# Kernel tuning notes

Hardware: AMD Instinct MI355X
Metric: run time of the kernel (lower is better)

Reference implementation:

```python
import jax, jax.numpy as jnp
import numpy as np

NP_, NA_ = 50000, 20000
D_IN, D_HID, D_OUT = 128, 128, 64
E_W, E_C, E_R = 250000, 500000, 250000


def setup_inputs() -> dict:
    key = jax.random.key(0)
    ks = jax.random.split(key, 14)
    s_in = 1.0 / np.sqrt(D_IN)
    s_h = 1.0 / np.sqrt(D_HID)
    return {
        "x_paper": jax.random.normal(ks[0], (NP_, D_IN), jnp.float32),
        "x_author": jax.random.normal(ks[1], (NA_, D_IN), jnp.float32),
        "Wl1": jax.random.normal(ks[2], (3, D_HID, D_IN), jnp.float32) * s_in,
        "bl1": jax.random.normal(ks[3], (3, D_HID), jnp.float32) * 0.01,
        "Wr1": jax.random.normal(ks[4], (3, D_HID, D_IN), jnp.float32) * s_in,
        "Wl2": jax.random.normal(ks[5], (3, D_OUT, D_HID), jnp.float32) * s_h,
        "bl2": jax.random.normal(ks[6], (3, D_OUT), jnp.float32) * 0.01,
        "Wr2": jax.random.normal(ks[7], (3, D_OUT, D_HID), jnp.float32) * s_h,
        "writes_src": jax.random.randint(ks[8], (E_W,), 0, NA_),
        "writes_dst": jax.random.randint(ks[9], (E_W,), 0, NP_),
        "cites_src": jax.random.randint(ks[10], (E_C,), 0, NP_),
        "cites_dst": jax.random.randint(ks[11], (E_C,), 0, NP_),
        "rev_src": jax.random.randint(ks[12], (E_R,), 0, NP_),
        "rev_dst": jax.random.randint(ks[13], (E_R,), 0, NA_),
    }


def _sage(x_src, x_dst, src, dst, Wl, bl, Wr, n_dst):
    # PyG SAGEConv(aggr='mean'): lin_l(mean_j x_src[j]) + lin_r(x_dst)
    agg = jax.ops.segment_sum(x_src[src], dst, num_segments=n_dst)
    cnt = jax.ops.segment_sum(jnp.ones_like(dst, dtype=x_src.dtype), dst,
                              num_segments=n_dst)
    agg = agg / jnp.maximum(cnt, 1.0)[:, None]  # degree-0 nodes -> 0 (PyG scatter-mean)
    return agg @ Wl.T + bl + x_dst @ Wr.T


def reference(x_paper, x_author, Wl1, bl1, Wr1, Wl2, bl2, Wr2,
              writes_src, writes_dst, cites_src, cites_dst, rev_src, rev_dst):
    def hetero_layer(xp, xa, Wl, bl, Wr):
        # HeteroConv(aggr='mean'): average per-relation outputs per dst node type
        op = 0.5 * (_sage(xa, xp, writes_src, writes_dst, Wl[0], bl[0], Wr[0], NP_)
                    + _sage(xp, xp, cites_src, cites_dst, Wl[1], bl[1], Wr[1], NP_))
        oa = _sage(xp, xa, rev_src, rev_dst, Wl[2], bl[2], Wr[2], NA_)
        return op, oa

    hp, ha = hetero_layer(x_paper, x_author, Wl1, bl1, Wr1)
    hp, ha = jax.nn.relu(hp), jax.nn.relu(ha)  # norm_type='none', dropout eval-mode
    hp, _ = hetero_layer(hp, ha, Wl2, bl2, Wr2)
    return hp  # logits for category='paper', [NP_, D_OUT]
```

## Files before the change

kernel.cpp:

```cpp
#include <hip/hip_runtime.h>

#define NP 50000
#define NA 20000
#define E_W 250000
#define E_C 500000
#define E_R 250000
#define E_TOT (E_W + E_C + E_R)
#define CAP 48
#define RBLK 4096
#define NSEG 245
#define PNODES 15000
#define CHK 500
#define NCH 30
#define NBIN 240

typedef __attribute__((ext_vector_type(8))) short short8;
typedef __attribute__((ext_vector_type(4))) float floatx4;
typedef __attribute__((ext_vector_type(2))) float floatx2;

__device__ __forceinline__ unsigned short f2bf(float f) {
    unsigned u = __float_as_uint(f);
    return (unsigned short)((u + 0x7FFFu + ((u >> 16) & 1u)) >> 16);
}
__device__ __forceinline__ float bflo(unsigned v) { return __uint_as_float(v << 16); }
__device__ __forceinline__ float bfhi(unsigned v) { return __uint_as_float(v & 0xFFFF0000u); }

__device__ __forceinline__ int node_idx(int node) {
    if (node < 2 * NP) {
        int rel1 = node >= NP;
        int d = node - (rel1 ? NP : 0);
        int p2 = d / 6250;
        return p2 * PNODES + (d - p2 * 6250) + (rel1 ? 6250 : 0);
    }
    int d = node - 2 * NP;
    int p2 = d / 2500;
    return p2 * PNODES + 12500 + (d - p2 * 2500);
}

__device__ __forceinline__ int frag_off(int NT, int j, int n, int k) {
    int t = n >> 4, ln = n & 15;
    int kb = k >> 5, q = (k >> 3) & 3, r = k & 7;
    return (((j * NT + t) * 4 + kb) * 64 + q * 16 + ln) * 8 + r;
}

__device__ __forceinline__ void prep_body(
    int idx,
    const float* __restrict__ xp, const float* __restrict__ xa,
    const float* __restrict__ Wl1, const float* __restrict__ Wr1,
    const float* __restrict__ Wl2, const float* __restrict__ Wr2,
    const float* __restrict__ bl1, const float* __restrict__ bl2,
    unsigned short* __restrict__ xpb, unsigned short* __restrict__ xab,
    unsigned* __restrict__ xp8, unsigned* __restrict__ xa8,
    unsigned short* __restrict__ Wp1, unsigned short* __restrict__ Wa1,
    unsigned short* __restrict__ Wt2, unsigned short* __restrict__ Wr2s,
    float* __restrict__ bias_p1, float* __restrict__ bias_a1,
    float* __restrict__ bias_p2) {
    const int n4p = NP * 32, n4a = NA * 32;
    if (idx < n4p + n4a) {
        const float* s; unsigned short* d; unsigned* d8; int i = idx;
        if (i < n4p) { s = xp; d = xpb; d8 = xp8; }
        else { s = xa; d = xab; d8 = xa8; i -= n4p; }
        float4 v = ((const float4*)s)[i];
        ushort4 u;
        u.x = f2bf(v.x); u.y = f2bf(v.y); u.z = f2bf(v.z); u.w = f2bf(v.w);
        ((ushort4*)d)[i] = u;
        int w = __builtin_amdgcn_cvt_pk_fp8_f32(v.x, v.y, 0, false);
        w = __builtin_amdgcn_cvt_pk_fp8_f32(v.z, v.w, w, true);
        d8[i] = (unsigned)w;
        return;
    }
    int j = idx - (n4p + n4a);
    if (j < 49152) {
        int jj = j >> 14, rem = j & 16383, n = rem >> 7, k = rem & 127;
        float v = (jj == 0)   ? 0.5f * Wl1[rem]
                  : (jj == 1) ? 0.5f * Wl1[16384 + rem]
                              : 0.5f * (Wr1[rem] + Wr1[16384 + rem]);
        Wp1[frag_off(8, jj, n, k)] = f2bf(v);
    } else if (j < 81920) {
        int i2 = j - 49152;
        int jj = i2 >> 14, rem = i2 & 16383, n = rem >> 7, k = rem & 127;
        float v = (jj == 0) ? Wl1[2 * 16384 + rem] : Wr1[2 * 16384 + rem];
        Wa1[frag_off(8, jj, n, k)] = f2bf(v);
    } else if (j < 98304) {
        int i2 = j - 81920;
        int jj = i2 >> 13, rem = i2 & 8191, n = rem >> 7, k = rem & 127;
        float v = 0.5f * Wl2[jj * 8192 + rem];
        Wt2[frag_off(4, jj, n, k)] = f2bf(v);
    } else if (j < 106496) {
        int i2 = j - 98304;
        int n = i2 >> 7, k = i2 & 127;
        float v = 0.5f * (Wr2[i2] + Wr2[8192 + i2]);
        Wr2s[frag_off(4, 0, n, k)] = f2bf(v);
    } else if (j < 106496 + 320) {
        int b = j - 106496;
        if (b < 128) bias_p1[b] = 0.5f * (bl1[b] + bl1[128 + b]);
        else if (b < 256) bias_a1[b - 128] = bl1[256 + b - 128];
        else bias_p2[b - 256] = 0.5f * (bl2[b - 256] + bl2[64 + b - 256]);
    }
}

__device__ __forceinline__ void edge_bin(
    int e, const int* __restrict__ w_src, const int* __restrict__ w_dst,
    const int* __restrict__ c_src, const int* __restrict__ c_dst,
    const int* __restrict__ r_src, const int* __restrict__ r_dst,
    int& bin, int& sub, int& src) {
    bool isC = (e >= E_W) & (e < E_W + E_C);
    bool isR = e >= E_W + E_C;
    const int* db = isR ? r_dst : (isC ? c_dst : w_dst);
    const int* sb = isR ? r_src : (isC ? c_src : w_src);
    int idx = e - (isC ? E_W : 0) - (isR ? (E_W + E_C) : 0);
    int d = db[idx];
    src = sb[idx];
    int p, local;
    if (isR) { p = d / 2500; local = 12500 + d - p * 2500; }
    else { p = d / 6250; local = (d - p * 6250) + (isC ? 6250 : 0); }
    int ch = local / CHK;
    bin = p * NCH + ch;
    sub = local - ch * CHK;
}

__device__ __forceinline__ void route_body(
    int bid, const int* __restrict__ w_src, const int* __restrict__ w_dst,
    const int* __restrict__ c_src, const int* __restrict__ c_dst,
    const int* __restrict__ r_src, const int* __restrict__ r_dst,
    unsigned* __restrict__ seg, int* __restrict__ segoff, int* __restrict__ segcnt,
    int* cnt_s, int* base_s, int* cur_s) {
    int tid = threadIdx.x, lane = tid & 63;
    for (int k = tid; k < NBIN; k += 256) cnt_s[k] = 0;
    __syncthreads();
#pragma unroll 4
    for (int u = 0; u < 16; ++u) {
        int e = bid * RBLK + u * 256 + tid;
        if (e < E_TOT) {
            int bin, sub, src;
            edge_bin(e, w_src, w_dst, c_src, c_dst, r_src, r_dst, bin, sub, src);
            atomicAdd(&cnt_s[bin], 1);
        }
    }
    __syncthreads();
    if (tid < 64) {
        int v[4], tot = 0;
#pragma unroll
        for (int q = 0; q < 4; ++q) {
            int k = tid * 4 + q;
            v[q] = (k < NBIN) ? cnt_s[k] : 0;
            tot += v[q];
        }
        int sc = tot;
#pragma unroll
        for (int ofs = 1; ofs < 64; ofs <<= 1) {
            int t = __shfl_up(sc, ofs, 64);
            if (lane >= ofs) sc += t;
        }
        int run = sc - tot;
#pragma unroll
        for (int q = 0; q < 4; ++q) {
            int k = tid * 4 + q;
            if (k < NBIN) { base_s[k] = run; run += v[q]; }
        }
    }
    __syncthreads();
    for (int k = tid; k < NBIN; k += 256) {
        segoff[bid * NBIN + k] = base_s[k];
        segcnt[bid * NBIN + k] = cnt_s[k];
        cur_s[k] = base_s[k];
    }
    __syncthreads();
    unsigned* segb = seg + (size_t)bid * RBLK;
#pragma unroll 4
    for (int u = 0; u < 16; ++u) {
        int e = bid * RBLK + u * 256 + tid;
        if (e < E_TOT) {
            int bin, sub, src;
            edge_bin(e, w_src, w_dst, c_src, c_dst, r_src, r_dst, bin, sub, src);
            int pos = atomicAdd(&cur_s[bin], 1);
            segb[pos] = (unsigned)src | ((unsigned)sub << 16);
        }
    }
}

__global__ __launch_bounds__(256) void route_prep(
    const float* xp, const float* xa, const float* Wl1, const float* Wr1,
    const float* Wl2, const float* Wr2, const float* bl1, const float* bl2,
    unsigned short* xpb, unsigned short* xab, unsigned* xp8, unsigned* xa8,
    unsigned short* Wp1, unsigned short* Wa1, unsigned short* Wt2, unsigned short* Wr2s,
    float* bias_p1, float* bias_a1, float* bias_p2,
    const int* w_src, const int* w_dst, const int* c_src, const int* c_dst,
    const int* r_src, const int* r_dst,
    unsigned* seg, int* segoff, int* segcnt) {
    __shared__ int cnt_s[NBIN], base_s[NBIN], cur_s[NBIN];
    if ((int)blockIdx.x < NSEG)
        route_body(blockIdx.x, w_src, w_dst, c_src, c_dst, r_src, r_dst,
                   seg, segoff, segcnt, cnt_s, base_s, cur_s);
    else
        prep_body((blockIdx.x - NSEG) * 256 + threadIdx.x, xp, xa, Wl1, Wr1, Wl2, Wr2,
                  bl1, bl2, xpb, xab, xp8, xa8, Wp1, Wa1, Wt2, Wr2s,
                  bias_p1, bias_a1, bias_p2);
}

__global__ __launch_bounds__(256) void fill2c(
    const unsigned* __restrict__ seg, const int* __restrict__ segoff,
    const int* __restrict__ segcnt, int* __restrict__ cnt,
    unsigned short* __restrict__ csr) {
    __shared__ unsigned short rows[CHK * CAP];
    __shared__ int cursor[CHK];
    __shared__ int offs[NSEG], cnts[NSEG];
    int k = blockIdx.x, tid = threadIdx.x;
    for (int s = tid; s < NSEG; s += 256) {
        offs[s] = segoff[s * NBIN + k];
        cnts[s] = segcnt[s * NBIN + k];
    }
    for (int l = tid; l < CHK; l += 256) cursor[l] = 0;
    __syncthreads();
    int grp = tid >> 4, gl = tid & 15;
    for (int s = grp; s < NSEG; s += 16) {
        int n = cnts[s];
        const unsigned* sp = seg + (size_t)s * RBLK + offs[s];
        for (int i = gl; i < n; i += 16) {
            unsigned v = sp[i];
            int sub = v >> 16, src = v & 0xFFFFu;
            int pos = atomicAdd(&cursor[sub], 1);
            if (pos < CAP) rows[sub * CAP + pos] = (unsigned short)src;
        }
    }
    __syncthreads();
    int p = k / NCH, ch = k - p * NCH;
    int gbase = p * PNODES + ch * CHK;
    for (int l = tid; l < CHK; l += 256) cnt[gbase + l] = cursor[l];
    const unsigned* rU = (const unsigned*)rows;
    unsigned* cU = (unsigned*)csr + (size_t)gbase * (CAP / 2);
    for (int i = tid; i < CHK * (CAP / 2); i += 256) cU[i] = rU[i];
}

__global__ void agg_pad(const unsigned* __restrict__ s0, unsigned short* __restrict__ d0,
                        const unsigned* __restrict__ s1, unsigned short* __restrict__ d1,
                        const unsigned* __restrict__ s2, unsigned short* __restrict__ d2,
                        const int* __restrict__ cnt, const unsigned short* __restrict__ csr) {
    int g = blockIdx.x * 8 + (threadIdx.x >> 5);
    int lane = threadIdx.x & 63;
    int sl = lane & 31, hw = lane & 32;
    const unsigned* sp; unsigned short* dst; int node, dummy;
    if (g < NP) { sp = s0; dst = d0; node = g; dummy = NA; }
    else if (g < 2 * NP) { sp = s1; dst = d1; node = g - NP; dummy = NP; }
    else if (g < 2 * NP + NA) { sp = s2; dst = d2; node = g - 2 * NP; dummy = NP; }
    else return;
    int idx = node_idx(g);
    int deg = cnt[idx];
    int degc = deg < CAP ? deg : CAP;
    const unsigned short* row = csr + (size_t)idx * CAP;
    int ei0 = (sl < degc) ? (int)row[sl] : dummy;
    int ei1 = (32 + sl < degc) ? (int)row[32 + sl] : dummy;
    int degw = degc;
    int other = __shfl_xor(degw, 32, 64);
    if (other > degw) degw = other;
    float a0 = 0.f, a1 = 0.f, a2 = 0.f, a3 = 0.f;
    float b0 = 0.f, b1 = 0.f, b2 = 0.f, b3 = 0.f;
    for (int i = 0; i < degw; i += 8) {
        unsigned v[8];
#pragma unroll
        for (int u = 0; u < 8; ++u) {
            int ii = i + u;
            int esrc = (ii < 32) ? ei0 : ei1;
            int qq = __shfl(esrc, hw | (ii & 31), 64);
            qq = (ii < degc) ? qq : dummy;
            v[u] = sp[(size_t)qq * 32 + sl];
        }
#pragma unroll
        for (int u = 0; u < 8; ++u) {
            floatx2 lo = __builtin_amdgcn_cvt_pk_f32_fp8(v[u], false);
            floatx2 hi = __builtin_amdgcn_cvt_pk_f32_fp8(v[u], true);
            if (u & 1) { b0 += lo.x; b1 += lo.y; b2 += hi.x; b3 += hi.y; }
            else       { a0 += lo.x; a1 += lo.y; a2 += hi.x; a3 += hi.y; }
        }
    }
    float scl = deg > 0 ? 1.f / (float)deg : 0.f;
    float r0 = (a0 + b0) * scl, r1 = (a1 + b1) * scl;
    float r2 = (a2 + b2) * scl, r3 = (a3 + b3) * scl;
    unsigned wlo = ((unsigned)f2bf(r1) << 16) | (unsigned)f2bf(r0);
    unsigned whi = ((unsigned)f2bf(r3) << 16) | (unsigned)f2bf(r2);
    ((uint2*)dst)[(size_t)node * 32 + sl] = make_uint2(wlo, whi);
}

__global__ void agg2(const unsigned short* __restrict__ ta, const unsigned short* __restrict__ tp,
                     const int* __restrict__ cnt, const unsigned short* __restrict__ csr,
                     float* __restrict__ aggF) {
    int node = blockIdx.x * 8 + (threadIdx.x >> 5);
    if (node >= NP) return;
    int lane = threadIdx.x & 63;
    int sl = lane & 31;
    int hw = lane & 32;
    int p2 = node / 6250;
    int base = p2 * PNODES + (node - p2 * 6250);
    float r0 = 0.f, r1 = 0.f;
#pragma unroll
    for (int rel = 0; rel < 2; ++rel) {
        int dummy = (rel == 0) ? NA : NP;
        const unsigned* sp = (const unsigned*)((rel == 0) ? ta : tp);
        int idx = base + (rel ? 6250 : 0);
        int deg = cnt[idx];
        int degc = deg < CAP ? deg : CAP;
        const unsigned short* row = csr + (size_t)idx * CAP;
        int ei0 = (sl < degc) ? (int)row[sl] : dummy;
        int ei1 = (32 + sl < degc) ? (int)row[32 + sl] : dummy;
        int degw = degc;
        int other = __shfl_xor(degw, 32, 64);
        if (other > degw) degw = other;
        float s0 = 0.f, s1 = 0.f, t0 = 0.f, t1 = 0.f;
        for (int i = 0; i < degw; i += 8) {
            unsigned v[8];
#pragma unroll
            for (int u = 0; u < 8; ++u) {
                int ii = i + u;
                int esrc = (ii < 32) ? ei0 : ei1;
                int qq = __shfl(esrc, hw | (ii & 31), 64);
                qq = (ii < degc) ? qq : dummy;
                v[u] = sp[(size_t)qq * 32 + sl];
            }
#pragma unroll
            for (int u = 0; u < 8; ++u) {
                if (u & 1) { t0 += bflo(v[u]); t1 += bfhi(v[u]); }
                else       { s0 += bflo(v[u]); s1 += bfhi(v[u]); }
            }
        }
        float scl = deg > 0 ? 1.f / (float)deg : 0.f;
        r0 += (s0 + t0) * scl; r1 += (s1 + t1) * scl;
    }
    ((float2*)aggF)[node * 32 + sl] = make_float2(r0, r1);
}

template <int J>
__device__ __forceinline__ void l1_core(
    const unsigned short* __restrict__ A0, const unsigned short* __restrict__ A1,
    const unsigned short* __restrict__ A2, const unsigned short* __restrict__ Wf,
    const float* __restrict__ bias, unsigned short* __restrict__ hout,
    const unsigned short* __restrict__ Wt, unsigned short* __restrict__ tout,
    unsigned short (*hT)[136], int M, int blk) {
    int tid = threadIdx.x;
    int wave = tid >> 6, lane = tid & 63;
    int ln = lane & 15, quad = lane >> 4;
    int row = blk * 64 + wave * 16 + ln;
    int rowc = row < M ? row : M - 1;
    const unsigned short* As[3] = {A0, A1, A2};
    floatx4 acc[8];
#pragma unroll
    for (int t = 0; t < 8; ++t) acc[t] = (floatx4){0.f, 0.f, 0.f, 0.f};
#pragma unroll
    for (int j = 0; j < J; ++j) {
        const unsigned short* A = As[j] + (long)rowc * 128 + quad * 8;
        const unsigned short* Wj = Wf + j * (128 * 128) + lane * 8;
#pragma unroll
        for (int kb = 0; kb < 4; ++kb) {
            short8 af = *(const short8*)(A + kb * 32);
#pragma unroll
            for (int t = 0; t < 8; ++t) {
                short8 bf = *(const short8*)(Wj + (t * 4 + kb) * 512);
                acc[t] = __builtin_amdgcn_mfma_f32_16x16x32_bf16(af, bf, acc[t], 0, 0, 0);
            }
        }
    }
    int orow0 = blk * 64 + wave * 16 + quad * 4;
    int lrow0 = wave * 16 + quad * 4;
#pragma unroll
    for (int t = 0; t < 8; ++t) {
        int col = t * 16 + ln;
        float bv = bias[col];
#pragma unroll
        for (int r = 0; r < 4; ++r) {
            float v = fmaxf(acc[t][r] + bv, 0.f);
            unsigned short hv = f2bf(v);
            hT[lrow0 + r][col] = hv;
            int orow = orow0 + r;
            if (hout != nullptr && orow < M) hout[(long)orow * 128 + col] = hv;
        }
    }
    __syncthreads();
    floatx4 tacc[4];
#pragma unroll
    for (int t = 0; t < 4; ++t) tacc[t] = (floatx4){0.f, 0.f, 0.f, 0.f};
#pragma unroll
    for (int kb = 0; kb < 4; ++kb) {
        short8 af = *(const short8*)&hT[wave * 16 + ln][quad * 8 + kb * 32];
#pragma unroll
        for (int t = 0; t < 4; ++t) {
            short8 bf = *(const short8*)(Wt + (t * 4 + kb) * 512 + lane * 8);
            tacc[t] = __builtin_amdgcn_mfma_f32_16x16x32_bf16(af, bf, tacc[t], 0, 0, 0);
        }
    }
#pragma unroll
    for (int t = 0; t < 4; ++t) {
        int col = t * 16 + ln;
#pragma unroll
        for (int r = 0; r < 4; ++r) {
            int orow = orow0 + r;
            if (orow < M) tout[(long)orow * 64 + col] = f2bf(tacc[t][r]);
        }
    }
}

__global__ __launch_bounds__(256) void gemm_l1f(
    const unsigned short* aggP1, const unsigned short* aggP2, const unsigned short* xpb,
    const unsigned short* Wp1, const float* bias_p1, unsigned short* hpb,
    const unsigned short* aggA, const unsigned short* xab,
    const unsigned short* Wa1, const float* bias_a1,
    const unsigned short* Wt2, unsigned short* ta, unsigned short* tp) {
    __shared__ unsigned short hT[64][136];
    constexpr int PB = (NP + 63) / 64;
    if ((int)blockIdx.x < PB)
        l1_core<3>(aggP1, aggP2, xpb, Wp1, bias_p1, hpb, Wt2 + 64 * 128, tp, hT, NP,
                   blockIdx.x);
    else
        l1_core<2>(aggA, xab, nullptr, Wa1, bias_a1, nullptr, Wt2, ta, hT, NA,
                   blockIdx.x - PB);
}

__global__ __launch_bounds__(256) void gemm_final(
    const unsigned short* __restrict__ hpb, const unsigned short* __restrict__ Wr2s,
    const float* __restrict__ bias_p2, const float* __restrict__ aggF,
    float* __restrict__ out) {
    int tid = threadIdx.x;
    int wave = tid >> 6, lane = tid & 63;
    int ln = lane & 15, quad = lane >> 4;
    int row = blockIdx.x * 64 + wave * 16 + ln;
    int rowc = row < NP ? row : NP - 1;
    floatx4 acc[4];
#pragma unroll
    for (int t = 0; t < 4; ++t) acc[t] = (floatx4){0.f, 0.f, 0.f, 0.f};
    const unsigned short* A = hpb + (long)rowc * 128 + quad * 8;
    const unsigned short* Wj = Wr2s + lane * 8;
#pragma unroll
    for (int kb = 0; kb < 4; ++kb) {
        short8 af = *(const short8*)(A + kb * 32);
#pragma unroll
        for (int t = 0; t < 4; ++t) {
            short8 bf = *(const short8*)(Wj + (t * 4 + kb) * 512);
            acc[t] = __builtin_amdgcn_mfma_f32_16x16x32_bf16(af, bf, acc[t], 0, 0, 0);
        }
    }
    int orow0 = blockIdx.x * 64 + wave * 16 + quad * 4;
#pragma unroll
    for (int t = 0; t < 4; ++t) {
        int col = t * 16 + ln;
        float bv = bias_p2[col];
#pragma unroll
        for (int r = 0; r < 4; ++r) {
            int orow = orow0 + r;
            if (orow < NP)
                out[(long)orow * 64 + col] = acc[t][r] + bv + aggF[(long)orow * 64 + col];
        }
    }
}

extern "C" void kernel_launch(void* const* d_in, const int* in_sizes, int n_in,
                              void* d_out, int out_size, void* d_ws, size_t ws_size,
                              hipStream_t stream) {
    (void)in_sizes; (void)n_in; (void)out_size; (void)ws_size;
    const float* xp  = (const float*)d_in[0];
    const float* xa  = (const float*)d_in[1];
    const float* Wl1 = (const float*)d_in[2];
    const float* bl1 = (const float*)d_in[3];
    const float* Wr1 = (const float*)d_in[4];
    const float* Wl2 = (const float*)d_in[5];
    const float* bl2 = (const float*)d_in[6];
    const float* Wr2 = (const float*)d_in[7];
    const int* w_src = (const int*)d_in[8];
    const int* w_dst = (const int*)d_in[9];
    const int* c_src = (const int*)d_in[10];
    const int* c_dst = (const int*)d_in[11];
    const int* r_src = (const int*)d_in[12];
    const int* r_dst = (const int*)d_in[13];
    float* out = (float*)d_out;

    char* p = (char*)d_ws;
    auto alloc = [&](size_t bytes) {
        char* r = p;
        p += (bytes + 255) & ~(size_t)255;
        return r;
    };
    unsigned short* xpb   = (unsigned short*)alloc((size_t)NP * 128 * 2);
    unsigned short* xab   = (unsigned short*)alloc((size_t)NA * 128 * 2);
    unsigned*       xp8   = (unsigned*)alloc((size_t)(NP + 1) * 128);
    unsigned*       xa8   = (unsigned*)alloc((size_t)(NA + 1) * 128);
    unsigned short* aggP1 = (unsigned short*)alloc((size_t)NP * 128 * 2);
    unsigned short* aggP2 = (unsigned short*)alloc((size_t)NP * 128 * 2);
    unsigned short* aggA  = (unsigned short*)alloc((size_t)NA * 128 * 2);
    unsigned short* hpb   = (unsigned short*)alloc((size_t)NP * 128 * 2);
    unsigned short* ta    = (unsigned short*)alloc((size_t)(NA + 1) * 64 * 2);
    unsigned short* tp    = (unsigned short*)alloc((size_t)(NP + 1) * 64 * 2);
    int*            cnt    = (int*)alloc((size_t)8 * PNODES * 4);
    unsigned short* csr    = (unsigned short*)alloc((size_t)8 * PNODES * CAP * 2);
    unsigned*       seg    = (unsigned*)alloc((size_t)NSEG * RBLK * 4);
    int*            segoff = (int*)alloc((size_t)NSEG * NBIN * 4);
    int*            segcnt = (int*)alloc((size_t)NSEG * NBIN * 4);
    unsigned short* Wp1  = (unsigned short*)alloc(3 * 128 * 128 * 2);
    unsigned short* Wa1  = (unsigned short*)alloc(2 * 128 * 128 * 2);
    unsigned short* Wt2  = (unsigned short*)alloc(2 * 64 * 128 * 2);
    unsigned short* Wr2s = (unsigned short*)alloc(64 * 128 * 2);
    float* bias_p1 = (float*)alloc(128 * 4);
    float* bias_a1 = (float*)alloc(128 * 4);
    float* bias_p2 = (float*)alloc(64 * 4);
    float* aggF = (float*)aggP2;

    hipMemsetAsync(xp8 + (size_t)NP * 32, 0, 128, stream);
    hipMemsetAsync(xa8 + (size_t)NA * 32, 0, 128, stream);
    hipMemsetAsync(ta + (size_t)NA * 64, 0, 128, stream);
    hipMemsetAsync(tp + (size_t)NP * 64, 0, 128, stream);

    int prep_threads = (NP + NA) * 32 + 106496 + 320;
    int prep_blocks = (prep_threads + 255) / 256;
    route_prep<<<NSEG + prep_blocks, 256, 0, stream>>>(
        xp, xa, Wl1, Wr1, Wl2, Wr2, bl1, bl2,
        xpb, xab, xp8, xa8, Wp1, Wa1, Wt2, Wr2s, bias_p1, bias_a1, bias_p2,
        w_src, w_dst, c_src, c_dst, r_src, r_dst, seg, segoff, segcnt);

    fill2c<<<NBIN, 256, 0, stream>>>(seg, segoff, segcnt, cnt, csr);

    agg_pad<<<(2 * NP + NA + 7) / 8, 256, 0, stream>>>(xa8, aggP1, xp8, aggP2, xp8, aggA,
                                                       cnt, csr);

    gemm_l1f<<<(NP + 63) / 64 + (NA + 63) / 64, 256, 0, stream>>>(
        aggP1, aggP2, xpb, Wp1, bias_p1, hpb, aggA, xab, Wa1, bias_a1, Wt2, ta, tp);

    agg2<<<(NP + 7) / 8, 256, 0, stream>>>(ta, tp, cnt, csr, aggF);
    gemm_final<<<(NP + 63) / 64, 256, 0, stream>>>(hpb, Wr2s, bias_p2, aggF, out);
}
```

Before: 229.8 us.

## Fuse layer-2 root GEMM into layer-1 GEMM and epilogue into agg2

The layer-2 self-term (h_paper @ Wr2) is now computed inside the layer-1 GEMM kernel from the shared-memory hidden tile, and written as fp32. The bias and self-term addition moves into the agg2 epilogue, so the gemm_final kernel and the bf16 hidden-state buffer go away. The GEMM tile also grows from 64 to 128 rows per block, with two row groups per wave reusing each weight fragment. This removes one launch and the write and reread of the hidden activations. In exchange it adds an fp32 intermediate (NP x 64), doubles the shared-memory tile, raises register pressure and halves the number of blocks.

```diff
diff --git a/kernel.cpp b/kernel.cpp
--- a/kernel.cpp
+++ b/kernel.cpp
@@ -283,7 +283,8 @@
 
 __global__ void agg2(const unsigned short* __restrict__ ta, const unsigned short* __restrict__ tp,
                      const int* __restrict__ cnt, const unsigned short* __restrict__ csr,
-                     float* __restrict__ aggF) {
+                     const float* __restrict__ sp_in, const float* __restrict__ bias_p2,
+                     float* __restrict__ out) {
     int node = blockIdx.x * 8 + (threadIdx.x >> 5);
     if (node >= NP) return;
     int lane = threadIdx.x & 63;
@@ -325,129 +326,117 @@
         float scl = deg > 0 ? 1.f / (float)deg : 0.f;
         r0 += (s0 + t0) * scl; r1 += (s1 + t1) * scl;
     }
-    ((float2*)aggF)[node * 32 + sl] = make_float2(r0, r1);
-}
-
-template <int J>
+    float2 spv = ((const float2*)sp_in)[(size_t)node * 32 + sl];
+    float2 bv = ((const float2*)bias_p2)[sl];
+    ((float2*)out)[(size_t)node * 32 + sl] =
+        make_float2(r0 + spv.x + bv.x, r1 + spv.y + bv.y);
+}
+
+template <int J, bool SP>
 __device__ __forceinline__ void l1_core(
     const unsigned short* __restrict__ A0, const unsigned short* __restrict__ A1,
     const unsigned short* __restrict__ A2, const unsigned short* __restrict__ Wf,
-    const float* __restrict__ bias, unsigned short* __restrict__ hout,
+    const float* __restrict__ bias,
     const unsigned short* __restrict__ Wt, unsigned short* __restrict__ tout,
+    const unsigned short* __restrict__ Wsp, float* __restrict__ spout,
     unsigned short (*hT)[136], int M, int blk) {
     int tid = threadIdx.x;
     int wave = tid >> 6, lane = tid & 63;
     int ln = lane & 15, quad = lane >> 4;
-    int row = blk * 64 + wave * 16 + ln;
-    int rowc = row < M ? row : M - 1;
+    int rbase = blk * 128 + wave * 32;
+    int rowc0 = rbase + ln;       if (rowc0 >= M) rowc0 = M - 1;
+    int rowc1 = rbase + 16 + ln;  if (rowc1 >= M) rowc1 = M - 1;
     const unsigned short* As[3] = {A0, A1, A2};
-    floatx4 acc[8];
-#pragma unroll
-    for (int t = 0; t < 8; ++t) acc[t] = (floatx4){0.f, 0.f, 0.f, 0.f};
+    floatx4 acc[2][8];
+#pragma unroll
+    for (int rg = 0; rg < 2; ++rg)
+#pragma unroll
+        for (int t = 0; t < 8; ++t) acc[rg][t] = (floatx4){0.f, 0.f, 0.f, 0.f};
 #pragma unroll
     for (int j = 0; j < J; ++j) {
-        const unsigned short* A = As[j] + (long)rowc * 128 + quad * 8;
+        const unsigned short* A = As[j];
+        const unsigned short* A0p = A + (long)rowc0 * 128 + quad * 8;
+        const unsigned short* A1p = A + (long)rowc1 * 128 + quad * 8;
         const unsigned short* Wj = Wf + j * (128 * 128) + lane * 8;
 #pragma unroll
         for (int kb = 0; kb < 4; ++kb) {
-            short8 af = *(const short8*)(A + kb * 32);
+            short8 af0 = *(const short8*)(A0p + kb * 32);
+            short8 af1 = *(const short8*)(A1p + kb * 32);
 #pragma unroll
             for (int t = 0; t < 8; ++t) {
                 short8 bf = *(const short8*)(Wj + (t * 4 + kb) * 512);
-                acc[t] = __builtin_amdgcn_mfma_f32_16x16x32_bf16(af, bf, acc[t], 0, 0, 0);
+                acc[0][t] = __builtin_amdgcn_mfma_f32_16x16x32_bf16(af0, bf, acc[0][t], 0, 0, 0);
+                acc[1][t] = __builtin_amdgcn_mfma_f32_16x16x32_bf16(af1, bf, acc[1][t], 0, 0, 0);
             }
         }
     }
-    int orow0 = blk * 64 + wave * 16 + quad * 4;
-    int lrow0 = wave * 16 + quad * 4;
-#pragma unroll
-    for (int t = 0; t < 8; ++t) {
-        int col = t * 16 + ln;
-        float bv = bias[col];
-#pragma unroll
-        for (int r = 0; r < 4; ++r) {
-            float v = fmaxf(acc[t][r] + bv, 0.f);
-            unsigned short hv = f2bf(v);
-            hT[lrow0 + r][col] = hv;
-            int orow = orow0 + r;
-            if (hout != nullptr && orow < M) hout[(long)orow * 128 + col] = hv;
-        }
-    }
-    __syncthreads();
-    floatx4 tacc[4];
-#pragma unroll
-    for (int t = 0; t < 4; ++t) tacc[t] = (floatx4){0.f, 0.f, 0.f, 0.f};
-#pragma unroll
-    for (int kb = 0; kb < 4; ++kb) {
-        short8 af = *(const short8*)&hT[wave * 16 + ln][quad * 8 + kb * 32];
+#pragma unroll
+    for (int rg = 0; rg < 2; ++rg) {
+        int lrow0 = wave * 32 + rg * 16 + quad * 4;
+#pragma unroll
+        for (int t = 0; t < 8; ++t) {
+            int col = t * 16 + ln;
+            float bv = bias[col];
+#pragma unroll
+            for (int r = 0; r < 4; ++r) {
+                float v = fmaxf(acc[rg][t][r] + bv, 0.f);
+                hT[lrow0 + r][col] = f2bf(v);
+            }
+        }
+    }
+    __syncthreads();
+#pragma unroll
+    for (int rg = 0; rg < 2; ++rg) {
+        floatx4 tacc[4], sacc[4];
 #pragma unroll
         for (int t = 0; t < 4; ++t) {
-            short8 bf = *(const short8*)(Wt + (t * 4 + kb) * 512 + lane * 8);
-            tacc[t] = __builtin_amdgcn_mfma_f32_16x16x32_bf16(af, bf, tacc[t], 0, 0, 0);
-        }
-    }
-#pragma unroll
-    for (int t = 0; t < 4; ++t) {
-        int col = t * 16 + ln;
-#pragma unroll
-        for (int r = 0; r < 4; ++r) {
-            int orow = orow0 + r;
-            if (orow < M) tout[(long)orow * 64 + col] = f2bf(tacc[t][r]);
+            tacc[t] = (floatx4){0.f, 0.f, 0.f, 0.f};
+            sacc[t] = (floatx4){0.f, 0.f, 0.f, 0.f};
+        }
+#pragma unroll
+        for (int kb = 0; kb < 4; ++kb) {
+            short8 af = *(const short8*)&hT[wave * 32 + rg * 16 + ln][quad * 8 + kb * 32];
+#pragma unroll
+            for (int t = 0; t < 4; ++t) {
+                short8 bf = *(const short8*)(Wt + (t * 4 + kb) * 512 + lane * 8);
+                tacc[t] = __builtin_amdgcn_mfma_f32_16x16x32_bf16(af, bf, tacc[t], 0, 0, 0);
+                if (SP) {
+                    short8 bs = *(const short8*)(Wsp + (t * 4 + kb) * 512 + lane * 8);
+                    sacc[t] = __builtin_amdgcn_mfma_f32_16x16x32_bf16(af, bs, sacc[t], 0, 0, 0);
+                }
+            }
+        }
+        int orow0 = blk * 128 + wave * 32 + rg * 16 + quad * 4;
+#pragma unroll
+        for (int t = 0; t < 4; ++t) {
+            int col = t * 16 + ln;
+#pragma unroll
+            for (int r = 0; r < 4; ++r) {
+                int orow = orow0 + r;
+                if (orow < M) {
+                    tout[(long)orow * 64 + col] = f2bf(tacc[t][r]);
+                    if (SP) spout[(long)orow * 64 + col] = sacc[t][r];
+                }
+            }
         }
     }
 }
 
 __global__ __launch_bounds__(256) void gemm_l1f(
     const unsigned short* aggP1, const unsigned short* aggP2, const unsigned short* xpb,
-    const unsigned short* Wp1, const float* bias_p1, unsigned short* hpb,
+    const unsigned short* Wp1, const float* bias_p1,
     const unsigned short* aggA, const unsigned short* xab,
     const unsigned short* Wa1, const float* bias_a1,
-    const unsigned short* Wt2, unsigned short* ta, unsigned short* tp) {
-    __shared__ unsigned short hT[64][136];
-    constexpr int PB = (NP + 63) / 64;
+    const unsigned short* Wt2, const unsigned short* Wr2s,
+    unsigned short* ta, unsigned short* tp, float* sp) {
+    __shared__ unsigned short hT[128][136];
+    constexpr int PB = (NP + 127) / 128;
     if ((int)blockIdx.x < PB)
-        l1_core<3>(aggP1, aggP2, xpb, Wp1, bias_p1, hpb, Wt2 + 64 * 128, tp, hT, NP,
-                   blockIdx.x);
+        l1_core<3, true>(aggP1, aggP2, xpb, Wp1, bias_p1, Wt2 + 64 * 128, tp, Wr2s, sp,
+                         hT, NP, blockIdx.x);
     else
-        l1_core<2>(aggA, xab, nullptr, Wa1, bias_a1, nullptr, Wt2, ta, hT, NA,
-                   blockIdx.x - PB);
-}
-
-__global__ __launch_bounds__(256) void gemm_final(
-    const unsigned short* __restrict__ hpb, const unsigned short* __restrict__ Wr2s,
-    const float* __restrict__ bias_p2, const float* __restrict__ aggF,
-    float* __restrict__ out) {
-    int tid = threadIdx.x;
-    int wave = tid >> 6, lane = tid & 63;
-    int ln = lane & 15, quad = lane >> 4;
-    int row = blockIdx.x * 64 + wave * 16 + ln;
-    int rowc = row < NP ? row : NP - 1;
-    floatx4 acc[4];
-#pragma unroll
-    for (int t = 0; t < 4; ++t) acc[t] = (floatx4){0.f, 0.f, 0.f, 0.f};
-    const unsigned short* A = hpb + (long)rowc * 128 + quad * 8;
-    const unsigned short* Wj = Wr2s + lane * 8;
-#pragma unroll
-    for (int kb = 0; kb < 4; ++kb) {
-        short8 af = *(const short8*)(A + kb * 32);
-#pragma unroll
-        for (int t = 0; t < 4; ++t) {
-            short8 bf = *(const short8*)(Wj + (t * 4 + kb) * 512);
-            acc[t] = __builtin_amdgcn_mfma_f32_16x16x32_bf16(af, bf, acc[t], 0, 0, 0);
-        }
-    }
-    int orow0 = blockIdx.x * 64 + wave * 16 + quad * 4;
-#pragma unroll
-    for (int t = 0; t < 4; ++t) {
-        int col = t * 16 + ln;
-        float bv = bias_p2[col];
-#pragma unroll
-        for (int r = 0; r < 4; ++r) {
-            int orow = orow0 + r;
-            if (orow < NP)
-                out[(long)orow * 64 + col] = acc[t][r] + bv + aggF[(long)orow * 64 + col];
-        }
-    }
+        l1_core<2, false>(aggA, xab, nullptr, Wa1, bias_a1, Wt2, ta, nullptr, nullptr,
+                          hT, NA, blockIdx.x - PB);
 }
 
 extern "C" void kernel_launch(void* const* d_in, const int* in_sizes, int n_in,
@@ -483,9 +472,9 @@
     unsigned short* aggP1 = (unsigned short*)alloc((size_t)NP * 128 * 2);
     unsigned short* aggP2 = (unsigned short*)alloc((size_t)NP * 128 * 2);
     unsigned short* aggA  = (unsigned short*)alloc((size_t)NA * 128 * 2);
-    unsigned short* hpb   = (unsigned short*)alloc((size_t)NP * 128 * 2);
     unsigned short* ta    = (unsigned short*)alloc((size_t)(NA + 1) * 64 * 2);
     unsigned short* tp    = (unsigned short*)alloc((size_t)(NP + 1) * 64 * 2);
+    float*          sp    = (float*)alloc((size_t)NP * 64 * 4);
     int*            cnt    = (int*)alloc((size_t)8 * PNODES * 4);
     unsigned short* csr    = (unsigned short*)alloc((size_t)8 * PNODES * CAP * 2);
     unsigned*       seg    = (unsigned*)alloc((size_t)NSEG * RBLK * 4);
@@ -498,7 +487,6 @@
     float* bias_p1 = (float*)alloc(128 * 4);
     float* bias_a1 = (float*)alloc(128 * 4);
     float* bias_p2 = (float*)alloc(64 * 4);
-    float* aggF = (float*)aggP2;
 
     hipMemsetAsync(xp8 + (size_t)NP * 32, 0, 128, stream);
     hipMemsetAsync(xa8 + (size_t)NA * 32, 0, 128, stream);
@@ -517,9 +505,8 @@
     agg_pad<<<(2 * NP + NA + 7) / 8, 256, 0, stream>>>(xa8, aggP1, xp8, aggP2, xp8, aggA,
                                                        cnt, csr);
 
-    gemm_l1f<<<(NP + 63) / 64 + (NA + 63) / 64, 256, 0, stream>>>(
-        aggP1, aggP2, xpb, Wp1, bias_p1, hpb, aggA, xab, Wa1, bias_a1, Wt2, ta, tp);
-
-    agg2<<<(NP + 7) / 8, 256, 0, stream>>>(ta, tp, cnt, csr, aggF);
-    gemm_final<<<(NP + 63) / 64, 256, 0, stream>>>(hpb, Wr2s, bias_p2, aggF, out);
-}
+    gemm_l1f<<<(NP + 127) / 128 + (NA + 127) / 128, 256, 0, stream>>>(
+        aggP1, aggP2, xpb, Wp1, bias_p1, aggA, xab, Wa1, bias_a1, Wt2, Wr2s, ta, tp, sp);
+
+    agg2<<<(NP + 7) / 8, 256, 0, stream>>>(ta, tp, cnt, csr, sp, bias_p2, out);
+}
```

Result: no change. 230.8 us (+0.4%).
